# Kernel optimization log

Hardware: AMD Instinct MI355X
Metric: run time of the kernel (lower is better)

Reference implementation:

```python
import jax, jax.numpy as jnp
import numpy as np

N = 20000      # nodes
E = 320000     # edges
F_IN = 64      # input_dim
HID = 128      # hidden_dim
H = 2          # heads (hard-coded in BGA)
G = 64         # num graphs (batch_step_dim[0])
MID = 32       # middle_dim
OUT = 1        # output_dim
EPS = 1e-5


def setup_inputs() -> dict:
    key = jax.random.key(0)
    ks = jax.random.split(key, 24)
    p = lambda k, shape: jax.random.normal(k, shape, jnp.float32) * 0.05
    inp = {}
    inp["x"] = jax.random.normal(ks[0], (N, F_IN), jnp.float32)
    inp["edge_index"] = jax.random.randint(ks[1], (2, E), 0, N)
    inp["atten_edge_index"] = jax.random.randint(ks[2], (2, E), 0, N)
    inp["batch_index"] = jnp.sort(jax.random.randint(ks[3], (N,), 0, G))
    # GANConv 0 MLP (2-layer: Linear->BN->ReLU->Linear)
    inp["g0_w1"] = p(ks[4], (F_IN, HID)); inp["g0_b1"] = jnp.zeros((HID,), jnp.float32)
    inp["g0_bn_g"] = jnp.ones((HID,), jnp.float32); inp["g0_bn_b"] = jnp.zeros((HID,), jnp.float32)
    inp["g0_w2"] = p(ks[5], (HID, HID)); inp["g0_b2"] = jnp.zeros((HID,), jnp.float32)
    # GANConv 1 MLP
    inp["g1_w1"] = p(ks[6], (HID, HID)); inp["g1_b1"] = jnp.zeros((HID,), jnp.float32)
    inp["g1_bn_g"] = jnp.ones((HID,), jnp.float32); inp["g1_bn_b"] = jnp.zeros((HID,), jnp.float32)
    inp["g1_w2"] = p(ks[7], (HID, HID)); inp["g1_b2"] = jnp.zeros((HID,), jnp.float32)
    # BGA batch norms after each GANConv
    inp["bn0_g"] = jnp.ones((HID,), jnp.float32); inp["bn0_b"] = jnp.zeros((HID,), jnp.float32)
    inp["bn1_g"] = jnp.ones((HID,), jnp.float32); inp["bn1_b"] = jnp.zeros((HID,), jnp.float32)
    # ATTConv atten_self: in=HID, out=HID, heads=2, concat=True
    inp["a1_wl"] = p(ks[8], (HID, H * HID)); inp["a1_bl"] = jnp.zeros((H * HID,), jnp.float32)
    inp["a1_wr"] = p(ks[9], (HID, H * HID)); inp["a1_br"] = jnp.zeros((H * HID,), jnp.float32)
    inp["a1_att"] = p(ks[10], (H, HID))
    inp["a1_bias"] = jnp.zeros((H * HID,), jnp.float32)
    # ATTConv atten: in=H*HID, out=HID, heads=2, concat=False (mean over heads)
    inp["a2_wl"] = p(ks[11], (H * HID, H * HID)); inp["a2_bl"] = jnp.zeros((H * HID,), jnp.float32)
    inp["a2_wr"] = p(ks[12], (H * HID, H * HID)); inp["a2_br"] = jnp.zeros((H * HID,), jnp.float32)
    inp["a2_att"] = p(ks[13], (H, HID))
    inp["a2_bias"] = jnp.zeros((HID,), jnp.float32)
    # prediction heads (only layer 0 and last are used)
    inp["pred0_w"] = p(ks[14], (F_IN, MID)); inp["pred0_b"] = jnp.zeros((MID,), jnp.float32)
    inp["predL_w"] = p(ks[15], (HID, MID)); inp["predL_b"] = jnp.zeros((MID,), jnp.float32)
    inp["out_w"] = p(ks[16], (MID, OUT)); inp["out_b"] = jnp.zeros((OUT,), jnp.float32)
    return inp


def _bn(x, g, b):  # training-mode batch norm over node axis
    m = x.mean(0)
    v = x.var(0)
    return (x - m) * jax.lax.rsqrt(v + EPS) * g + b


def _mlp2(x, w1, b1, bn_g, bn_b, w2, b2):
    h = jax.nn.relu(_bn(x @ w1 + b1, bn_g, bn_b))
    return h @ w2 + b2


def _gan_conv(x, edge_index, w1, b1, bn_g, bn_b, w2, b2):
    row, col = edge_index[0], edge_index[1]
    agg = jax.ops.segment_sum(x[col], row, num_segments=x.shape[0])
    return _mlp2(x + agg, w1, b1, bn_g, bn_b, w2, b2)


def _att_conv(x, edge_index, wl, bl, wr, br, att, bias, concat):
    # GATv2-style: e = leaky_relu(x_i + x_j); alpha = softmax_dst(<e, att>)
    n = x.shape[0]
    xl = (x @ wl + bl).reshape(n, H, HID)  # source proj
    xr = (x @ wr + br).reshape(n, H, HID)  # target proj
    src, dst = edge_index[0], edge_index[1]
    e = jax.nn.leaky_relu(xl[src] + xr[dst], 0.2)          # [E,H,C]
    logit = jnp.einsum('ehc,hc->eh', e, att)               # [E,H]
    lmax = jax.ops.segment_max(logit, dst, num_segments=n)
    w = jnp.exp(logit - lmax[dst])
    denom = jax.ops.segment_sum(w, dst, num_segments=n)
    alpha = w / (denom[dst] + 1e-16)                       # [E,H]
    out = jax.ops.segment_sum(xl[src] * alpha[:, :, None], dst, num_segments=n)
    if concat:
        out = out.reshape(n, H * HID)
    else:
        out = out.mean(1)
    return out + bias, alpha


def reference(x, edge_index, atten_edge_index, batch_index,
              g0_w1, g0_b1, g0_bn_g, g0_bn_b, g0_w2, g0_b2,
              g1_w1, g1_b1, g1_bn_g, g1_bn_b, g1_w2, g1_b2,
              bn0_g, bn0_b, bn1_g, bn1_b,
              a1_wl, a1_bl, a1_wr, a1_br, a1_att, a1_bias,
              a2_wl, a2_bl, a2_wr, a2_br, a2_att, a2_bias,
              pred0_w, pred0_b, predL_w, predL_b, out_w, out_b):
    h0 = x
    h1 = jax.nn.relu(_bn(_gan_conv(h0, edge_index, g0_w1, g0_b1, g0_bn_g, g0_bn_b, g0_w2, g0_b2), bn0_g, bn0_b))
    h2 = jax.nn.relu(_bn(_gan_conv(h1, edge_index, g1_w1, g1_b1, g1_bn_g, g1_bn_b, g1_w2, g1_b2), bn1_g, bn1_b))
    emb, _ = _att_conv(h2, edge_index, a1_wl, a1_bl, a1_wr, a1_br, a1_att, a1_bias, concat=True)
    emb = jax.nn.relu(emb)
    atten_out, alpha = _att_conv(emb, atten_edge_index, a2_wl, a2_bl, a2_wr, a2_br, a2_att, a2_bias, concat=False)
    atten_out = jax.nn.relu(atten_out)
    pool0 = jax.ops.segment_sum(h0, batch_index, num_segments=G)
    poolL = jax.ops.segment_sum(atten_out, batch_index, num_segments=G)
    out_h = jax.nn.relu((pool0 @ pred0_w + pred0_b) + (poolL @ predL_w + predL_b))
    outputs = out_h @ out_w + out_b
    return (outputs, atten_out, alpha)
```

## Files before the change

kernel.cpp:

```cpp
#include <hip/hip_runtime.h>
#include <hip/hip_bf16.h>

#define N_NODES 20000
#define E_EDGES 320000
#define F_INN   64
#define HID     128
#define HEADS   2
#define HC      (HEADS * HID)
#define G_GR    64
#define MIDD    32
#define EPSV    1e-5f
#define NBUK    79

#define CDIV(a, b) (((a) + (b) - 1) / (b))

typedef __attribute__((ext_vector_type(8))) short          bf16x8;
typedef __attribute__((ext_vector_type(4))) float          f32x4;
typedef __attribute__((ext_vector_type(8))) unsigned short u16x8;

__device__ inline float bf2f(unsigned short u) { return __uint_as_float((unsigned)u << 16); }
__device__ inline unsigned short f2bf(float f) {
    unsigned u = __float_as_uint(f);
    unsigned r = u + 0x7FFFu + ((u >> 16) & 1u);
    return (unsigned short)(r >> 16);
}

struct Csr3 {
    const int* key[3];
    const int* other[3];
    int* btot;
    int* bstart;
    int* bcur;
    int* rowptr[3];
    int* out[3];
    int2* tmp;
};

__global__ __launch_bounds__(256) void k_bhist(Csr3 c) {
    __shared__ int hist[NBUK];
    const int y = blockIdx.y;
    const int chunk0 = blockIdx.x * 4096;
    const int t = threadIdx.x;
    for (int i = t; i < NBUK; i += 256) hist[i] = 0;
    __syncthreads();
#pragma unroll
    for (int i = 0; i < 16; i++) {
        int e = chunk0 + (i << 8) + t;
        if (e < E_EDGES) atomicAdd(&hist[c.key[y][e] >> 8], 1);
    }
    __syncthreads();
    for (int i = t; i < NBUK; i += 256)
        if (hist[i] > 0) atomicAdd(&c.btot[y * NBUK + i], hist[i]);
}

__global__ void k_bscan(Csr3 c) {
    __shared__ int sh[3 * NBUK];
    int t = threadIdx.x;
    for (int i = t; i < 3 * NBUK; i += 256) sh[i] = c.btot[i];
    __syncthreads();
    if (t < 3) {
        int run = 0;
        int* bs = c.bstart + t * (NBUK + 1);
        for (int b = 0; b < NBUK; b++) {
            bs[b] = run;
            c.bcur[t * NBUK + b] = run;
            run += sh[t * NBUK + b];
        }
        bs[NBUK] = run;
    }
}

__global__ __launch_bounds__(256) void k_bucketA(Csr3 c) {
    __shared__ int hist[NBUK], base[NBUK], off[NBUK];
    const int y = blockIdx.y;
    const int chunk0 = blockIdx.x * 4096;
    const int t = threadIdx.x;
    for (int i = t; i < NBUK; i += 256) { hist[i] = 0; off[i] = 0; }
    __syncthreads();
    int keys[16], vals[16], bks[16];
#pragma unroll
    for (int i = 0; i < 16; i++) {
        int e = chunk0 + (i << 8) + t;
        bool ok = (e < E_EDGES);
        int k = ok ? c.key[y][e] : 0;
        keys[i] = k;
        vals[i] = ok ? ((y == 2) ? e : c.other[y][e]) : 0;
        bks[i] = ok ? (k >> 8) : -1;
        if (ok) atomicAdd(&hist[k >> 8], 1);
    }
    __syncthreads();
    if (t < NBUK && hist[t] > 0) base[t] = atomicAdd(&c.bcur[y * NBUK + t], hist[t]);
    __syncthreads();
    int2* ty = c.tmp + (size_t)y * E_EDGES;
#pragma unroll
    for (int i = 0; i < 16; i++) {
        int b = bks[i];
        if (b >= 0) {
            int o = atomicAdd(&off[b], 1);
            ty[base[b] + o] = make_int2(keys[i], vals[i]);
        }
    }
}

__global__ __launch_bounds__(256) void k_bucketB(Csr3 c) {
    __shared__ int cnt[256], lbase[256], run[256];
    const int y = blockIdx.y;
    const int b = blockIdx.x;
    const int nbase = b << 8;
    const int t = threadIdx.x;
    cnt[t] = 0; run[t] = 0;
    __syncthreads();
    const int bs = c.bstart[y * (NBUK + 1) + b];
    const int be = c.bstart[y * (NBUK + 1) + b + 1];
    const int2* ty = c.tmp + (size_t)y * E_EDGES;
    for (int i = bs + t; i < be; i += 256)
        atomicAdd(&cnt[ty[i].x - nbase], 1);
    __syncthreads();
    int v = cnt[t];
    lbase[t] = v;
    __syncthreads();
    for (int off = 1; off < 256; off <<= 1) {
        int u = (t >= off) ? lbase[t - off] : 0;
        __syncthreads();
        lbase[t] += u;
        __syncthreads();
    }
    int excl = lbase[t] - v;
    __syncthreads();
    lbase[t] = excl;
    __syncthreads();
    int n = nbase + t;
    if (n < N_NODES) c.rowptr[y][n] = bs + excl;
    if (b == NBUK - 1 && t == 0) c.rowptr[y][N_NODES] = E_EDGES;
    int* outy = c.out[y];
    for (int i = bs + t; i < be; i += 256) {
        int2 kv = ty[i];
        int k = kv.x - nbase;
        int o = atomicAdd(&run[k], 1);
        outy[bs + lbase[k] + o] = kv.y;
    }
}

__global__ __launch_bounds__(256) void k_gather_f32(const float4* __restrict__ x,
                                                    const int* __restrict__ rowptr,
                                                    const int* __restrict__ srcs,
                                                    unsigned short* __restrict__ z) {
    int gid = blockIdx.x * blockDim.x + threadIdx.x;
    int n = gid >> 4;
    if (n >= N_NODES) return;
    int q = gid & 15;
    float4 acc = x[((size_t)n << 4) + q];
    int p1 = rowptr[n + 1];
    for (int p = rowptr[n]; p < p1; p++) {
        float4 v = x[((size_t)srcs[p] << 4) + q];
        acc.x += v.x; acc.y += v.y; acc.z += v.z; acc.w += v.w;
    }
    ushort4 o;
    o.x = f2bf(acc.x); o.y = f2bf(acc.y); o.z = f2bf(acc.z); o.w = f2bf(acc.w);
    *(ushort4*)&z[((size_t)n << 6) + (q << 2)] = o;
}

__global__ __launch_bounds__(256) void k_gather_bn(const u16x8* __restrict__ raw,
                                                   const int* __restrict__ rowptr,
                                                   const int* __restrict__ srcs,
                                                   const float* __restrict__ bn_sums,
                                                   const float* __restrict__ g,
                                                   const float* __restrict__ b,
                                                   u16x8* __restrict__ z) {
    int gid = blockIdx.x * blockDim.x + threadIdx.x;
    int n = gid >> 4;
    if (n >= N_NODES) return;
    int q = gid & 15;
    float sc[8], sh[8];
#pragma unroll
    for (int i = 0; i < 8; i++) {
        int c = (q << 3) + i;
        float mean = bn_sums[c] / N_NODES;
        float istd = rsqrtf(bn_sums[HID + c] / N_NODES - mean * mean + EPSV);
        float s = istd * g[c];
        sc[i] = s;
        sh[i] = b[c] - mean * s;
    }
    u16x8 u0 = raw[((size_t)n << 4) + q];
    float acc[8];
#pragma unroll
    for (int i = 0; i < 8; i++) acc[i] = fmaxf(bf2f(u0[i]) * sc[i] + sh[i], 0.f);
    int p1 = rowptr[n + 1];
    for (int p = rowptr[n]; p < p1; p++) {
        u16x8 v = raw[((size_t)srcs[p] << 4) + q];
#pragma unroll
        for (int i = 0; i < 8; i++) acc[i] += fmaxf(bf2f(v[i]) * sc[i] + sh[i], 0.f);
    }
    u16x8 o;
#pragma unroll
    for (int i = 0; i < 8; i++) o[i] = f2bf(acc[i]);
    z[((size_t)n << 4) + q] = o;
}

struct WtJob  { const float* src; unsigned short* dst; int K; int N; };
struct WtJobs { WtJob j[8]; };
__global__ void k_wt_cast(WtJobs jobs) {
    WtJob jb = jobs.j[blockIdx.y];
    int total = jb.K * jb.N;
    for (int i = blockIdx.x * blockDim.x + threadIdx.x; i < total; i += gridDim.x * blockDim.x) {
        int nn = i / jb.K, kk = i - nn * jb.K;
        jb.dst[i] = f2bf(jb.src[(size_t)kk * jb.N + nn]);
    }
}

template <int STATS, int BNA, int TM, int BIAS2>
__global__ __launch_bounds__(256) void k_mfma_gemm(const unsigned short* __restrict__ A,
                                                   const unsigned short* __restrict__ Wt,
                                                   const float* __restrict__ biasL,
                                                   const float* __restrict__ biasR,
                                                   unsigned short* __restrict__ Cout,
                                                   int M, int K, int N,
                                                   float* __restrict__ stats_sums,
                                                   const float* __restrict__ bn_sums,
                                                   const float* __restrict__ bn_g,
                                                   const float* __restrict__ bn_b) {
    constexpr int BNF = (TM == 128) ? 4 : 2;
    __shared__ unsigned short As[TM][40];
    __shared__ unsigned short Bs[128][40];
    __shared__ float s_scale[BNA ? HID : 1], s_shift[BNA ? HID : 1];
    const int t = threadIdx.x;
    if (BNA) {
        if (t < HID) {
            float mean = bn_sums[t] / M;
            float istd = rsqrtf(bn_sums[HID + t] / M - mean * mean + EPSV);
            float s = istd * bn_g[t];
            s_scale[t] = s;
            s_shift[t] = bn_b[t] - mean * s;
        }
        __syncthreads();
    }
    const int wave = t >> 6, lane = t & 63;
    const int row0 = blockIdx.y * TM, col0 = blockIdx.x * 128;
    const int wm = (TM == 128) ? ((wave & 1) << 6) : 0;
    const int wn = (TM == 128) ? ((wave >> 1) << 6) : (wave << 5);
    const int lm = lane & 15, lk = (lane >> 4) << 3;
    constexpr int APASS = TM / 64;
    f32x4 acc[4][BNF] = {};
    for (int k0 = 0; k0 < K; k0 += 32) {
        u16x8 av[APASS], wv[2];
#pragma unroll
        for (int i = 0; i < APASS; i++) {
            int c = t + (i << 8);
            int r = c >> 2, ko = (c & 3) << 3;
            u16x8 zv = {};
            int gr = row0 + r;
            av[i] = (gr < M) ? *(const u16x8*)&A[(size_t)gr * K + k0 + ko] : zv;
            if (BNA) {
#pragma unroll
                for (int j = 0; j < 8; j++) {
                    int kc = k0 + ko + j;
                    float v = fmaxf(bf2f(av[i][j]) * s_scale[kc] + s_shift[kc], 0.f);
                    av[i][j] = f2bf(v);
                }
            }
        }
#pragma unroll
        for (int i = 0; i < 2; i++) {
            int c = t + (i << 8);
            int r = c >> 2, ko = (c & 3) << 3;
            wv[i] = *(const u16x8*)&Wt[(size_t)(col0 + r) * K + k0 + ko];
        }
        __syncthreads();
#pragma unroll
        for (int i = 0; i < APASS; i++) {
            int c = t + (i << 8);
            int r = c >> 2, ko = (c & 3) << 3;
            *(u16x8*)&As[r][ko] = av[i];
        }
#pragma unroll
        for (int i = 0; i < 2; i++) {
            int c = t + (i << 8);
            int r = c >> 2, ko = (c & 3) << 3;
            *(u16x8*)&Bs[r][ko] = wv[i];
        }
        __syncthreads();
        bf16x8 af[4], bfm[BNF];
#pragma unroll
        for (int i = 0; i < 4; i++) af[i]  = *(const bf16x8*)&As[wm + (i << 4) + lm][lk];
#pragma unroll
        for (int j = 0; j < BNF; j++) bfm[j] = *(const bf16x8*)&Bs[wn + (j << 4) + lm][lk];
#pragma unroll
        for (int i = 0; i < 4; i++)
#pragma unroll
            for (int j = 0; j < BNF; j++)
                acc[i][j] = __builtin_amdgcn_mfma_f32_16x16x32_bf16(af[i], bfm[j], acc[i][j], 0, 0, 0);
    }
    const int lr4 = (lane >> 4) << 2;
    float s1[BNF], s2[BNF];
#pragma unroll
    for (int j = 0; j < BNF; j++) { s1[j] = 0.f; s2[j] = 0.f; }
#pragma unroll
    for (int j = 0; j < BNF; j++) {
        int col = col0 + wn + (j << 4) + lm;
        float bv = BIAS2 ? ((col < 256) ? biasL[col] : biasR[col - 256]) : biasL[col];
#pragma unroll
        for (int i = 0; i < 4; i++) {
#pragma unroll
            for (int r = 0; r < 4; r++) {
                int row = row0 + wm + (i << 4) + lr4 + r;
                if (row < M) {
                    float v = acc[i][j][r] + bv;
                    Cout[(size_t)row * N + col] = f2bf(v);
                    if (STATS) { s1[j] += v; s2[j] += v * v; }
                }
            }
        }
    }
    if (STATS) {
#pragma unroll
        for (int j = 0; j < BNF; j++) {
            s1[j] += __shfl_xor(s1[j], 16, 64); s1[j] += __shfl_xor(s1[j], 32, 64);
            s2[j] += __shfl_xor(s2[j], 16, 64); s2[j] += __shfl_xor(s2[j], 32, 64);
        }
        if ((lane >> 4) == 0) {
#pragma unroll
            for (int j = 0; j < BNF; j++) {
                int col = col0 + wn + (j << 4) + lm;
                atomicAdd(&stats_sums[col], s1[j]);
                atomicAdd(&stats_sums[HID + col], s2[j]);
            }
        }
    }
}

#define ATT_CAP 192
template <int CONCAT, int WITH_ALPHA>
__global__ __launch_bounds__(256) void k_att_fused(const ushort4* __restrict__ Q,
                                                   const int* __restrict__ rowptr,
                                                   const int* __restrict__ plist,
                                                   const int* __restrict__ other,
                                                   const float* __restrict__ att,
                                                   const float* __restrict__ bias,
                                                   void* __restrict__ outp,
                                                   float* __restrict__ alpha_out) {
    __shared__ float s_lg[4][ATT_CAP][2];
    const int t = threadIdx.x;
    const int wave = t >> 6, l = t & 63;
    const int n = blockIdx.x * 4 + wave;
    const int h = l >> 5;
    ushort4 ur = Q[((size_t)n << 7) + 64 + l];
    float xr4[4] = {bf2f(ur.x), bf2f(ur.y), bf2f(ur.z), bf2f(ur.w)};
    const float* ap = &att[h * HID + ((l & 31) << 2)];
    float at4[4] = {ap[0], ap[1], ap[2], ap[3]};
    const int p0 = rowptr[n], p1 = rowptr[n + 1];

    float m = -INFINITY, ssum = 0.f;
    float acc[4] = {0.f, 0.f, 0.f, 0.f};

#define ATT_SRC(p) (WITH_ALPHA ? other[plist[p]] : plist[p])

#define ATT_LOGIT(uv, x4, tl) do { \
        x4[0] = bf2f(uv.x); x4[1] = bf2f(uv.y); x4[2] = bf2f(uv.z); x4[3] = bf2f(uv.w); \
        float v0 = x4[0] + xr4[0]; v0 = (v0 > 0.f) ? v0 : 0.2f * v0; \
        float v1 = x4[1] + xr4[1]; v1 = (v1 > 0.f) ? v1 : 0.2f * v1; \
        float v2 = x4[2] + xr4[2]; v2 = (v2 > 0.f) ? v2 : 0.2f * v2; \
        float v3 = x4[3] + xr4[3]; v3 = (v3 > 0.f) ? v3 : 0.2f * v3; \
        tl = at4[0] * v0 + at4[1] * v1 + at4[2] * v2 + at4[3] * v3; \
    } while (0)

#define ATT_ONLINE(x4, tl, idx) do { \
        float mn = fmaxf(m, tl); \
        float sc = __expf(m - mn); \
        float w  = __expf(tl - mn); \
        ssum = ssum * sc + w; \
        acc[0] = acc[0] * sc + w * x4[0]; \
        acc[1] = acc[1] * sc + w * x4[1]; \
        acc[2] = acc[2] * sc + w * x4[2]; \
        acc[3] = acc[3] * sc + w * x4[3]; \
        m = mn; \
        if (WITH_ALPHA && (idx) < ATT_CAP && (l & 31) == 0) s_lg[wave][idx][h] = tl; \
    } while (0)

    int p = p0;
    for (; p + 4 <= p1; p += 4) {
        float x4[4][4], tl[4];
        ushort4 uv[4];
        int ss[4];
#pragma unroll
        for (int j = 0; j < 4; j++) ss[j] = ATT_SRC(p + j);
#pragma unroll
        for (int j = 0; j < 4; j++) uv[j] = Q[((size_t)ss[j] << 7) + l];
#pragma unroll
        for (int j = 0; j < 4; j++) ATT_LOGIT(uv[j], x4[j], tl[j]);
#pragma unroll
        for (int k = 1; k <= 16; k <<= 1) {
#pragma unroll
            for (int j = 0; j < 4; j++) tl[j] += __shfl_xor(tl[j], k, 64);
        }
        if (WITH_ALPHA && (l & 31) == 0) {
#pragma unroll
            for (int j = 0; j < 4; j++)
                if (p + j - p0 < ATT_CAP) s_lg[wave][p + j - p0][h] = tl[j];
        }
        float tmax = fmaxf(fmaxf(tl[0], tl[1]), fmaxf(tl[2], tl[3]));
        float mn = fmaxf(m, tmax);
        float sc = __expf(m - mn);
        float w0 = __expf(tl[0] - mn), w1 = __expf(tl[1] - mn);
        float w2 = __expf(tl[2] - mn), w3 = __expf(tl[3] - mn);
        ssum = ssum * sc + (w0 + w1 + w2 + w3);
#pragma unroll
        for (int c = 0; c < 4; c++)
            acc[c] = acc[c] * sc + w0 * x4[0][c] + w1 * x4[1][c] + w2 * x4[2][c] + w3 * x4[3][c];
        m = mn;
    }
    for (; p < p1; p++) {
        float x4[4], tl;
        ushort4 uv = Q[((size_t)ATT_SRC(p) << 7) + l];
        ATT_LOGIT(uv, x4, tl);
#pragma unroll
        for (int k = 1; k <= 16; k <<= 1) tl += __shfl_xor(tl, k, 64);
        ATT_ONLINE(x4, tl, p - p0);
    }
    float inv = 1.f / (ssum + 1e-16f);

    if (WITH_ALPHA) {
        float m_o   = __shfl_xor(m, 32, 64);
        float inv_o = __shfl_xor(inv, 32, 64);
        float m2[2], i2[2];
        m2[h] = m; m2[1 - h] = m_o;
        i2[h] = inv; i2[1 - h] = inv_o;
        int cnt = p1 - p0;
        int ccnt = (cnt < ATT_CAP) ? cnt : ATT_CAP;
        for (int i = l; i < ccnt * 2; i += 64) {
            int idx = i >> 1, hh = i & 1;
            float a = __expf(s_lg[wave][idx][hh] - m2[hh]) * i2[hh];
            alpha_out[plist[p0 + idx] * HEADS + hh] = a;
        }
        for (int pp = p0 + ATT_CAP; pp < p1; pp++) {
            float x4[4], tl;
            ushort4 uv = Q[((size_t)ATT_SRC(pp) << 7) + l];
            ATT_LOGIT(uv, x4, tl);
#pragma unroll
            for (int k = 1; k <= 16; k <<= 1) tl += __shfl_xor(tl, k, 64);
            if ((l & 31) == 0) alpha_out[plist[pp] * HEADS + h] = __expf(tl - m) * inv;
        }
    }

    if (CONCAT) {
        const float* bp = &bias[l << 2];
        ushort4 o;
        o.x = f2bf(fmaxf(acc[0] * inv + bp[0], 0.f));
        o.y = f2bf(fmaxf(acc[1] * inv + bp[1], 0.f));
        o.z = f2bf(fmaxf(acc[2] * inv + bp[2], 0.f));
        o.w = f2bf(fmaxf(acc[3] * inv + bp[3], 0.f));
        ((ushort4*)outp)[((size_t)n << 6) + l] = o;
    } else {
        float o[4];
#pragma unroll
        for (int i = 0; i < 4; i++) {
            float v = acc[i] * inv;
            float other_v = __shfl_xor(v, 32, 64);
            o[i] = 0.5f * (v + other_v);
        }
        if (l < 32) {
            const float* bp = &bias[(l & 31) << 2];
            float4 ov;
            ov.x = fmaxf(o[0] + bp[0], 0.f); ov.y = fmaxf(o[1] + bp[1], 0.f);
            ov.z = fmaxf(o[2] + bp[2], 0.f); ov.w = fmaxf(o[3] + bp[3], 0.f);
            ((float4*)outp)[((size_t)n << 5) + l] = ov;
        }
    }
#undef ATT_SRC
#undef ATT_LOGIT
#undef ATT_ONLINE
}

template <int C>
__global__ __launch_bounds__(256) void k_pool_atomic(const float* __restrict__ X,
                                                     const int* __restrict__ batch,
                                                     float* __restrict__ pool, int npb) {
    const int RP = 256 / C;
    int c = threadIdx.x & (C - 1);
    int rofs = threadIdx.x / C;
    int i0 = blockIdx.x * npb;
    int i1 = min(i0 + npb, N_NODES);
    float acc = 0.f;
    int gcur = -1;
    for (int i = i0 + rofs; i < i1; i += RP) {
        int g = batch[i];
        if (g != gcur) {
            if (gcur >= 0) atomicAdd(&pool[gcur * C + c], acc);
            acc = 0.f; gcur = g;
        }
        acc += X[(size_t)i * C + c];
    }
    if (gcur >= 0) atomicAdd(&pool[gcur * C + c], acc);
}

__global__ void k_head(const float* __restrict__ pool0, const float* __restrict__ poolL,
                       const float* __restrict__ p0w, const float* __restrict__ p0b,
                       const float* __restrict__ pLw, const float* __restrict__ pLb,
                       const float* __restrict__ ow, const float* __restrict__ ob,
                       float* __restrict__ outputs) {
    int g = blockIdx.x;
    int m = threadIdx.x;
    __shared__ float sh[MIDD];
    if (m < MIDD) {
        float s = p0b[m] + pLb[m];
        for (int k = 0; k < F_INN; k++) s += pool0[g * F_INN + k] * p0w[k * MIDD + m];
        for (int k = 0; k < HID; k++)  s += poolL[g * HID + k] * pLw[k * MIDD + m];
        sh[m] = fmaxf(s, 0.f);
    }
    __syncthreads();
    if (m == 0) {
        float s = ob[0];
        for (int k = 0; k < MIDD; k++) s += sh[k] * ow[k];
        outputs[g] = s;
    }
}

extern "C" void kernel_launch(void* const* d_in, const int* in_sizes, int n_in,
                              void* d_out, int out_size, void* d_ws, size_t ws_size,
                              hipStream_t stream) {
    const float* x      = (const float*)d_in[0];
    const int*   ei     = (const int*)d_in[1];
    const int*   aei    = (const int*)d_in[2];
    const int*   batch  = (const int*)d_in[3];
    const float* g0_w1  = (const float*)d_in[4];
    const float* g0_b1  = (const float*)d_in[5];
    const float* g0_bng = (const float*)d_in[6];
    const float* g0_bnb = (const float*)d_in[7];
    const float* g0_w2  = (const float*)d_in[8];
    const float* g0_b2  = (const float*)d_in[9];
    const float* g1_w1  = (const float*)d_in[10];
    const float* g1_b1  = (const float*)d_in[11];
    const float* g1_bng = (const float*)d_in[12];
    const float* g1_bnb = (const float*)d_in[13];
    const float* g1_w2  = (const float*)d_in[14];
    const float* g1_b2  = (const float*)d_in[15];
    const float* bn0_g  = (const float*)d_in[16];
    const float* bn0_b  = (const float*)d_in[17];
    const float* bn1_g  = (const float*)d_in[18];
    const float* bn1_b  = (const float*)d_in[19];
    const float* a1_wl  = (const float*)d_in[20];
    const float* a1_bl  = (const float*)d_in[21];
    const float* a1_wr  = (const float*)d_in[22];
    const float* a1_br  = (const float*)d_in[23];
    const float* a1_att = (const float*)d_in[24];
    const float* a1_bias= (const float*)d_in[25];
    const float* a2_wl  = (const float*)d_in[26];
    const float* a2_bl  = (const float*)d_in[27];
    const float* a2_wr  = (const float*)d_in[28];
    const float* a2_br  = (const float*)d_in[29];
    const float* a2_att = (const float*)d_in[30];
    const float* a2_bias= (const float*)d_in[31];
    const float* p0w    = (const float*)d_in[32];
    const float* p0b    = (const float*)d_in[33];
    const float* pLw    = (const float*)d_in[34];
    const float* pLb    = (const float*)d_in[35];
    const float* ow     = (const float*)d_in[36];
    const float* ob     = (const float*)d_in[37];

    float* out_head  = (float*)d_out;
    float* atten_out = out_head + G_GR;
    float* alpha_out = atten_out + (size_t)N_NODES * HID;

    float* ws = (float*)d_ws;
    float* sums4 = ws;
    float* pool0 = sums4 + 4 * 256;
    float* poolL = pool0 + G_GR * F_INN;
    int*   btot  = (int*)(poolL + G_GR * HID);
    const size_t zero_bytes = (4 * 256 + G_GR * F_INN + G_GR * HID + 3 * NBUK) * 4;

    int* ip = btot + 3 * NBUK;
    int* bstart = ip; ip += 3 * (NBUK + 1);
    int* bcur   = ip; ip += 3 * NBUK;
    int* rowptr[3]; int* payload[3];
    for (int c = 0; c < 3; c++) {
        rowptr[c]  = ip; ip += N_NODES + 1;
        payload[c] = ip; ip += E_EDGES;
    }
    int2* tmp3 = (int2*)ip; ip += 2 * 3 * E_EDGES;
    const size_t NB = (size_t)N_NODES * HC;
    unsigned short* B1 = (unsigned short*)ip;
    unsigned short* B2 = B1 + NB;
    unsigned short* Qb = B2 + NB;
    unsigned short* g0w1t = Qb + 2 * NB;
    unsigned short* g0w2t = g0w1t + 128 * 64;
    unsigned short* g1w1t = g0w2t + 128 * 128;
    unsigned short* g1w2t = g1w1t + 128 * 128;
    unsigned short* a1wlt = g1w2t + 128 * 128;
    unsigned short* a1wrt = a1wlt + 256 * 128;
    unsigned short* a2wlt = a1wrt + 256 * 128;
    unsigned short* a2wrt = a2wlt + 256 * 256;

    const int* e_row = ei;
    const int* e_col = ei + E_EDGES;
    const int* a_src = aei;
    const int* a_dst = aei + E_EDGES;

    const int TB = 256;
#define GRID1(n) dim3(CDIV((n), TB))

    {
        WtJobs jobs;
        jobs.j[0] = {g0_w1, g0w1t, F_INN, HID};
        jobs.j[1] = {g0_w2, g0w2t, HID,   HID};
        jobs.j[2] = {g1_w1, g1w1t, HID,   HID};
        jobs.j[3] = {g1_w2, g1w2t, HID,   HID};
        jobs.j[4] = {a1_wl, a1wlt, HID,   HC};
        jobs.j[5] = {a1_wr, a1wrt, HID,   HC};
        jobs.j[6] = {a2_wl, a2wlt, HC,    HC};
        jobs.j[7] = {a2_wr, a2wrt, HC,    HC};
        k_wt_cast<<<dim3(32, 8), TB, 0, stream>>>(jobs);
    }

    hipMemsetAsync(sums4, 0, zero_bytes, stream);
    {
        Csr3 c;
        c.key[0] = e_row; c.other[0] = e_col;
        c.key[1] = e_col; c.other[1] = e_row;
        c.key[2] = a_dst; c.other[2] = a_src;
        c.btot = btot; c.bstart = bstart; c.bcur = bcur; c.tmp = tmp3;
        for (int i = 0; i < 3; i++) { c.rowptr[i] = rowptr[i]; c.out[i] = payload[i]; }
        k_bhist<<<dim3(CDIV(E_EDGES, 4096), 3), TB, 0, stream>>>(c);
        k_bscan<<<dim3(1), TB, 0, stream>>>(c);
        k_bucketA<<<dim3(CDIV(E_EDGES, 4096), 3), TB, 0, stream>>>(c);
        k_bucketB<<<dim3(NBUK, 3), TB, 0, stream>>>(c);
    }

    const dim3 gemm_g1(1, CDIV(N_NODES, 64));
    const dim3 gemm_gq(4, CDIV(N_NODES, 128));
    const float* NOF = nullptr;

    k_gather_f32<<<GRID1(N_NODES * 16), TB, 0, stream>>>((const float4*)x, rowptr[0], payload[0], B1);
    k_mfma_gemm<1, 0, 64, 0><<<gemm_g1, TB, 0, stream>>>(B1, g0w1t, g0_b1, NOF, B2, N_NODES, F_INN, HID,
                                                         sums4 + 0, NOF, NOF, NOF);
    k_mfma_gemm<1, 1, 64, 0><<<gemm_g1, TB, 0, stream>>>(B2, g0w2t, g0_b2, NOF, B1, N_NODES, HID, HID,
                                                         sums4 + 256, sums4 + 0, g0_bng, g0_bnb);

    k_gather_bn<<<GRID1(N_NODES * 16), TB, 0, stream>>>((const u16x8*)B1, rowptr[0], payload[0],
                                                        sums4 + 256, bn0_g, bn0_b, (u16x8*)B2);
    k_mfma_gemm<1, 0, 64, 0><<<gemm_g1, TB, 0, stream>>>(B2, g1w1t, g1_b1, NOF, B1, N_NODES, HID, HID,
                                                         sums4 + 512, NOF, NOF, NOF);
    k_mfma_gemm<1, 1, 64, 0><<<gemm_g1, TB, 0, stream>>>(B1, g1w2t, g1_b2, NOF, B2, N_NODES, HID, HID,
                                                         sums4 + 768, sums4 + 512, g1_bng, g1_bnb);

    k_mfma_gemm<0, 1, 128, 1><<<gemm_gq, TB, 0, stream>>>(B2, a1wlt, a1_bl, a1_br, Qb, N_NODES, HID, 512,
                                                          nullptr, sums4 + 768, bn1_g, bn1_b);
    k_att_fused<1, 0><<<dim3(N_NODES / 4), TB, 0, stream>>>(
        (const ushort4*)Qb, rowptr[1], payload[1], nullptr, a1_att, a1_bias, (void*)B1, nullptr);

    k_mfma_gemm<0, 0, 128, 1><<<gemm_gq, TB, 0, stream>>>(B1, a2wlt, a2_bl, a2_br, Qb, N_NODES, HC, 512,
                                                          nullptr, NOF, NOF, NOF);
    k_att_fused<0, 1><<<dim3(N_NODES / 4), TB, 0, stream>>>(
        (const ushort4*)Qb, rowptr[2], payload[2], a_src, a2_att, a2_bias, (void*)atten_out, alpha_out);

    {
        const int npb = 64;
        k_pool_atomic<F_INN><<<dim3(CDIV(N_NODES, npb)), TB, 0, stream>>>(x, batch, pool0, npb);
        k_pool_atomic<HID><<<dim3(CDIV(N_NODES, npb)), TB, 0, stream>>>(atten_out, batch, poolL, npb);
    }
    k_head<<<dim3(G_GR), 64, 0, stream>>>(pool0, poolL, p0w, p0b, pLw, pLb, ow, ob, out_head);
}
```

Measured before the change: 446.0 us.

## Split attention edges across two waves per node and unroll gather loops

The attention kernel now gives each destination node two waves. Each wave runs an online softmax over half of the node's edges, and the two partial states (max, sum, accumulators) are merged through shared memory after a block barrier. Both gather kernels unroll their edge loops by four with independent loads, so more memory requests are in flight. The split doubles the number of active waves for the latency-bound attention gather, at the cost of a __syncthreads, extra shared memory, and the second wave sitting idle during the epilogue.

```diff
diff --git a/kernel.cpp b/kernel.cpp
--- a/kernel.cpp
+++ b/kernel.cpp
@@ -150,11 +150,24 @@
     if (n >= N_NODES) return;
     int q = gid & 15;
     float4 acc = x[((size_t)n << 4) + q];
-    int p1 = rowptr[n + 1];
-    for (int p = rowptr[n]; p < p1; p++) {
+    float4 a1 = make_float4(0.f, 0.f, 0.f, 0.f), a2 = a1, a3 = a1;
+    int p = rowptr[n], p1 = rowptr[n + 1];
+    for (; p + 4 <= p1; p += 4) {
+        float4 v0 = x[((size_t)srcs[p + 0] << 4) + q];
+        float4 v1 = x[((size_t)srcs[p + 1] << 4) + q];
+        float4 v2 = x[((size_t)srcs[p + 2] << 4) + q];
+        float4 v3 = x[((size_t)srcs[p + 3] << 4) + q];
+        acc.x += v0.x; acc.y += v0.y; acc.z += v0.z; acc.w += v0.w;
+        a1.x += v1.x; a1.y += v1.y; a1.z += v1.z; a1.w += v1.w;
+        a2.x += v2.x; a2.y += v2.y; a2.z += v2.z; a2.w += v2.w;
+        a3.x += v3.x; a3.y += v3.y; a3.z += v3.z; a3.w += v3.w;
+    }
+    for (; p < p1; p++) {
         float4 v = x[((size_t)srcs[p] << 4) + q];
         acc.x += v.x; acc.y += v.y; acc.z += v.z; acc.w += v.w;
     }
+    acc.x += a1.x + a2.x + a3.x; acc.y += a1.y + a2.y + a3.y;
+    acc.z += a1.z + a2.z + a3.z; acc.w += a1.w + a2.w + a3.w;
     ushort4 o;
     o.x = f2bf(acc.x); o.y = f2bf(acc.y); o.z = f2bf(acc.z); o.w = f2bf(acc.w);
     *(ushort4*)&z[((size_t)n << 6) + (q << 2)] = o;
@@ -185,8 +198,21 @@
     float acc[8];
 #pragma unroll
     for (int i = 0; i < 8; i++) acc[i] = fmaxf(bf2f(u0[i]) * sc[i] + sh[i], 0.f);
-    int p1 = rowptr[n + 1];
-    for (int p = rowptr[n]; p < p1; p++) {
+    int p = rowptr[n], p1 = rowptr[n + 1];
+    for (; p + 4 <= p1; p += 4) {
+        u16x8 v0 = raw[((size_t)srcs[p + 0] << 4) + q];
+        u16x8 v1 = raw[((size_t)srcs[p + 1] << 4) + q];
+        u16x8 v2 = raw[((size_t)srcs[p + 2] << 4) + q];
+        u16x8 v3 = raw[((size_t)srcs[p + 3] << 4) + q];
+#pragma unroll
+        for (int i = 0; i < 8; i++) {
+            acc[i] += fmaxf(bf2f(v0[i]) * sc[i] + sh[i], 0.f)
+                    + fmaxf(bf2f(v1[i]) * sc[i] + sh[i], 0.f)
+                    + fmaxf(bf2f(v2[i]) * sc[i] + sh[i], 0.f)
+                    + fmaxf(bf2f(v3[i]) * sc[i] + sh[i], 0.f);
+        }
+    }
+    for (; p < p1; p++) {
         u16x8 v = raw[((size_t)srcs[p] << 4) + q];
 #pragma unroll
         for (int i = 0; i < 8; i++) acc[i] += fmaxf(bf2f(v[i]) * sc[i] + sh[i], 0.f);
@@ -338,16 +364,23 @@
                                                    const float* __restrict__ bias,
                                                    void* __restrict__ outp,
                                                    float* __restrict__ alpha_out) {
-    __shared__ float s_lg[4][ATT_CAP][2];
+    __shared__ float s_lg[WITH_ALPHA ? 2 : 1][WITH_ALPHA ? ATT_CAP : 1][2];
+    __shared__ float comb[2][64][6];
     const int t = threadIdx.x;
     const int wave = t >> 6, l = t & 63;
-    const int n = blockIdx.x * 4 + wave;
+    const int nl = wave >> 1;
+    const int half = wave & 1;
+    const int n = blockIdx.x * 2 + nl;
     const int h = l >> 5;
     ushort4 ur = Q[((size_t)n << 7) + 64 + l];
     float xr4[4] = {bf2f(ur.x), bf2f(ur.y), bf2f(ur.z), bf2f(ur.w)};
     const float* ap = &att[h * HID + ((l & 31) << 2)];
     float at4[4] = {ap[0], ap[1], ap[2], ap[3]};
-    const int p0 = rowptr[n], p1 = rowptr[n + 1];
+    const int p0n = rowptr[n], p1n = rowptr[n + 1];
+    const int cnt = p1n - p0n;
+    const int mid = p0n + (cnt >> 1);
+    const int my0 = half ? mid : p0n;
+    const int my1 = half ? p1n : mid;
 
     float m = -INFINITY, ssum = 0.f;
     float acc[4] = {0.f, 0.f, 0.f, 0.f};
@@ -363,21 +396,8 @@
         tl = at4[0] * v0 + at4[1] * v1 + at4[2] * v2 + at4[3] * v3; \
     } while (0)
 
-#define ATT_ONLINE(x4, tl, idx) do { \
-        float mn = fmaxf(m, tl); \
-        float sc = __expf(m - mn); \
-        float w  = __expf(tl - mn); \
-        ssum = ssum * sc + w; \
-        acc[0] = acc[0] * sc + w * x4[0]; \
-        acc[1] = acc[1] * sc + w * x4[1]; \
-        acc[2] = acc[2] * sc + w * x4[2]; \
-        acc[3] = acc[3] * sc + w * x4[3]; \
-        m = mn; \
-        if (WITH_ALPHA && (idx) < ATT_CAP && (l & 31) == 0) s_lg[wave][idx][h] = tl; \
-    } while (0)
-
-    int p = p0;
-    for (; p + 4 <= p1; p += 4) {
+    int p = my0;
+    for (; p + 4 <= my1; p += 4) {
         float x4[4][4], tl[4];
         ushort4 uv[4];
         int ss[4];
@@ -395,7 +415,7 @@
         if (WITH_ALPHA && (l & 31) == 0) {
 #pragma unroll
             for (int j = 0; j < 4; j++)
-                if (p + j - p0 < ATT_CAP) s_lg[wave][p + j - p0][h] = tl[j];
+                if (p + j - p0n < ATT_CAP) s_lg[nl][p + j - p0n][h] = tl[j];
         }
         float tmax = fmaxf(fmaxf(tl[0], tl[1]), fmaxf(tl[2], tl[3]));
         float mn = fmaxf(m, tmax);
@@ -408,13 +428,39 @@
             acc[c] = acc[c] * sc + w0 * x4[0][c] + w1 * x4[1][c] + w2 * x4[2][c] + w3 * x4[3][c];
         m = mn;
     }
-    for (; p < p1; p++) {
+    for (; p < my1; p++) {
         float x4[4], tl;
         ushort4 uv = Q[((size_t)ATT_SRC(p) << 7) + l];
         ATT_LOGIT(uv, x4, tl);
 #pragma unroll
         for (int k = 1; k <= 16; k <<= 1) tl += __shfl_xor(tl, k, 64);
-        ATT_ONLINE(x4, tl, p - p0);
+        float mn = fmaxf(m, tl);
+        float sc = __expf(m - mn);
+        float w  = __expf(tl - mn);
+        ssum = ssum * sc + w;
+#pragma unroll
+        for (int c = 0; c < 4; c++) acc[c] = acc[c] * sc + w * x4[c];
+        m = mn;
+        if (WITH_ALPHA && (p - p0n) < ATT_CAP && (l & 31) == 0) s_lg[nl][p - p0n][h] = tl;
+    }
+
+    if (half == 1) {
+        comb[nl][l][0] = m; comb[nl][l][1] = ssum;
+        comb[nl][l][2] = acc[0]; comb[nl][l][3] = acc[1];
+        comb[nl][l][4] = acc[2]; comb[nl][l][5] = acc[3];
+    }
+    __syncthreads();
+    if (half == 1) return;
+    {
+        float m2v = comb[nl][l][0], s2v = comb[nl][l][1];
+        float mm = fmaxf(m, m2v);
+        float sc1 = (m   > -INFINITY) ? __expf(m   - mm) : 0.f;
+        float sc2 = (m2v > -INFINITY) ? __expf(m2v - mm) : 0.f;
+        ssum = ssum * sc1 + s2v * sc2;
+#pragma unroll
+        for (int c = 0; c < 4; c++)
+            acc[c] = acc[c] * sc1 + comb[nl][l][2 + c] * sc2;
+        m = mm;
     }
     float inv = 1.f / (ssum + 1e-16f);
 
@@ -424,14 +470,13 @@
         float m2[2], i2[2];
         m2[h] = m; m2[1 - h] = m_o;
         i2[h] = inv; i2[1 - h] = inv_o;
-        int cnt = p1 - p0;
         int ccnt = (cnt < ATT_CAP) ? cnt : ATT_CAP;
         for (int i = l; i < ccnt * 2; i += 64) {
             int idx = i >> 1, hh = i & 1;
-            float a = __expf(s_lg[wave][idx][hh] - m2[hh]) * i2[hh];
-            alpha_out[plist[p0 + idx] * HEADS + hh] = a;
-        }
-        for (int pp = p0 + ATT_CAP; pp < p1; pp++) {
+            float a = __expf(s_lg[nl][idx][hh] - m2[hh]) * i2[hh];
+            alpha_out[plist[p0n + idx] * HEADS + hh] = a;
+        }
+        for (int pp = p0n + ATT_CAP; pp < p1n; pp++) {
             float x4[4], tl;
             ushort4 uv = Q[((size_t)ATT_SRC(pp) << 7) + l];
             ATT_LOGIT(uv, x4, tl);
@@ -467,7 +512,6 @@
     }
 #undef ATT_SRC
 #undef ATT_LOGIT
-#undef ATT_ONLINE
 }
 
 template <int C>
@@ -643,12 +687,12 @@
 
     k_mfma_gemm<0, 1, 128, 1><<<gemm_gq, TB, 0, stream>>>(B2, a1wlt, a1_bl, a1_br, Qb, N_NODES, HID, 512,
                                                           nullptr, sums4 + 768, bn1_g, bn1_b);
-    k_att_fused<1, 0><<<dim3(N_NODES / 4), TB, 0, stream>>>(
+    k_att_fused<1, 0><<<dim3(N_NODES / 2), TB, 0, stream>>>(
         (const ushort4*)Qb, rowptr[1], payload[1], nullptr, a1_att, a1_bias, (void*)B1, nullptr);
 
     k_mfma_gemm<0, 0, 128, 1><<<gemm_gq, TB, 0, stream>>>(B1, a2wlt, a2_bl, a2_br, Qb, N_NODES, HC, 512,
                                                           nullptr, NOF, NOF, NOF);
-    k_att_fused<0, 1><<<dim3(N_NODES / 4), TB, 0, stream>>>(
+    k_att_fused<0, 1><<<dim3(N_NODES / 2), TB, 0, stream>>>(
         (const ushort4*)Qb, rowptr[2], payload[2], a_src, a2_att, a2_bias, (void*)atten_out, alpha_out);
 
     {
```

Result: no change. 454.3 us (+1.9%).
